# Optimization experiments

Hardware: AMD Instinct MI355X
Metric: run time of the kernel (lower is better)

Reference implementation:

```python
import jax, jax.numpy as jnp
import numpy as np

B, D = 65536, 1024
E, U, T = 10, 10, 2  # experts, expert units, tasks


def setup_inputs() -> dict:
    key = jax.random.key(0)
    ks = jax.random.split(key, 8)
    s = 0.02
    return {
        "x": jax.random.normal(ks[0], (B, D), dtype=jnp.float32),
        "show_index": jax.random.randint(ks[1], (B,), 0, 100),
        "st": jax.random.normal(ks[2], (B, 16), dtype=jnp.float32),
        "expert_w": jax.random.normal(ks[3], (E, D, U), dtype=jnp.float32) * s,
        "expert_b": jnp.zeros((E, U), dtype=jnp.float32),
        "gate_w": jax.random.normal(ks[4], (T, D, E), dtype=jnp.float32) * s,
        "gate_b": jnp.zeros((T, E), dtype=jnp.float32),
        "ctr_w": jax.random.normal(ks[5], (U, 1), dtype=jnp.float32) * s,
        "ctr_b": jnp.zeros((1,), dtype=jnp.float32),
        "cvr_w": jax.random.normal(ks[6], (U, 1), dtype=jnp.float32) * s,
        "cvr_b": jnp.zeros((1,), dtype=jnp.float32),
    }


def reference(x, show_index, st, expert_w, expert_b, gate_w, gate_b,
              ctr_w, ctr_b, cvr_w, cvr_b):
    # experts_output[b, u, e] = relu(x @ W_e + b_e)  (stacked on axis 2)
    experts_output = jax.nn.relu(
        jnp.einsum("bd,edu->bue", x, expert_w) + expert_b.T[None, :, :]
    )  # [B, U, E]
    # gates[b, t, e] = softmax over experts
    gates = jax.nn.softmax(
        jnp.einsum("bd,tde->bte", x, gate_w) + gate_b[None, :, :], axis=-1
    )  # [B, T, E]
    # weighted sum over experts for each task: [B, T, U]
    task_inputs = jnp.einsum("bue,bte->btu", experts_output, gates)
    ctr_logits = jax.nn.sigmoid(task_inputs[:, 0, :] @ ctr_w + ctr_b)  # [B, 1]
    cvr_logits = jax.nn.sigmoid(task_inputs[:, 1, :] @ cvr_w + cvr_b)  # [B, 1]
    return (ctr_logits, cvr_logits)
```

## Files before the change

### kernel.cpp

```cpp
#include <hip/hip_runtime.h>
#include <hip/hip_bf16.h>

#define B_ROWS 65536
#define D_DIM  1024
#define NC     120
#define NCP    128
#define MBLK   64
#define BK     64
#define ASTR   72
#define CSTR   121

typedef __attribute__((ext_vector_type(4))) float f32x4;
typedef __attribute__((ext_vector_type(8))) short bf16x8;

__device__ __forceinline__ unsigned short f2bf(float f) {
  union { float f; unsigned u; } v; v.f = f;
  unsigned r = v.u + 0x7FFFu + ((v.u >> 16) & 1u);
  return (unsigned short)(r >> 16);
}

__global__ __launch_bounds__(256) void pack_w(const float* __restrict__ ew,
                                              const float* __restrict__ gw,
                                              short* __restrict__ wt) {
  int idx = blockIdx.x * 256 + threadIdx.x;
  int c = idx >> 10, d = idx & 1023;
  float v = 0.f;
  if (c < 100) {
    int e = c / 10, u = c % 10;
    v = ew[(e * D_DIM + d) * 10 + u];
  } else if (c < NC) {
    int q = c - 100; int t = q / 10, e = q % 10;
    v = gw[(t * D_DIM + d) * 10 + e];
  }
  wt[c * D_DIM + d] = (short)f2bf(v);
}

union Smem {
  struct { short A[MBLK * ASTR]; short Bm[NCP * ASTR]; } s;
  float C[MBLK * CSTR];
};

__global__ __launch_bounds__(256) void mmoe_main(
    const float* __restrict__ x, const short* __restrict__ wt,
    const float* __restrict__ eb, const float* __restrict__ gb,
    const float* __restrict__ ctr_w, const float* __restrict__ ctr_b,
    const float* __restrict__ cvr_w, const float* __restrict__ cvr_b,
    float* __restrict__ out) {
  __shared__ Smem sm;
  const int tid  = threadIdx.x;
  const int wave = tid >> 6, lane = tid & 63;
  const int m0   = blockIdx.x * MBLK;

  const int arow = tid >> 4;
  const int akp  = (tid & 15) * 4;
  const int bc   = tid >> 3;
  const int bks  = (tid & 7) * 8;

  const int lhi = lane >> 4;
  const int llo = lane & 15;

  f32x4 acc[8];
  const f32x4 vzero = {0.f, 0.f, 0.f, 0.f};
  #pragma unroll
  for (int i = 0; i < 8; ++i) acc[i] = vzero;

  for (int k0 = 0; k0 < D_DIM; k0 += BK) {
    __syncthreads();
    #pragma unroll
    for (int j = 0; j < 4; ++j) {
      const int row = j * 16 + arow;
      const float4 v = *reinterpret_cast<const float4*>(
          x + (size_t)(m0 + row) * D_DIM + k0 + akp);
      ushort4 h;
      h.x = f2bf(v.x); h.y = f2bf(v.y); h.z = f2bf(v.z); h.w = f2bf(v.w);
      *reinterpret_cast<ushort4*>(&sm.s.A[row * ASTR + akp]) = h;
    }
    #pragma unroll
    for (int j = 0; j < 4; ++j) {
      const int c = j * 32 + bc;
      const uint4 v = *reinterpret_cast<const uint4*>(wt + c * D_DIM + k0 + bks);
      *reinterpret_cast<uint4*>(&sm.s.Bm[c * ASTR + bks]) = v;
    }
    __syncthreads();
    #pragma unroll
    for (int ks = 0; ks < BK; ks += 32) {
      const bf16x8 af = *reinterpret_cast<const bf16x8*>(
          &sm.s.A[(wave * 16 + llo) * ASTR + ks + lhi * 8]);
      #pragma unroll
      for (int ct = 0; ct < 8; ++ct) {
        const bf16x8 bf = *reinterpret_cast<const bf16x8*>(
            &sm.s.Bm[(ct * 16 + llo) * ASTR + ks + lhi * 8]);
        acc[ct] = __builtin_amdgcn_mfma_f32_16x16x32_bf16(af, bf, acc[ct], 0, 0, 0);
      }
    }
  }

  __syncthreads();
  #pragma unroll
  for (int ct = 0; ct < 8; ++ct) {
    const int col = ct * 16 + llo;
    if (col < NC) {
      #pragma unroll
      for (int r = 0; r < 4; ++r) {
        const int row = wave * 16 + lhi * 4 + r;
        sm.C[row * CSTR + col] = acc[ct][r];
      }
    }
  }
  __syncthreads();

  if (tid < MBLK) {
    const float* crow = &sm.C[tid * CSTR];
    float w0[10], w1[10];
    #pragma unroll
    for (int u = 0; u < 10; ++u) { w0[u] = ctr_w[u]; w1[u] = cvr_w[u]; }
    float s0[10], s1[10];
    #pragma unroll
    for (int e = 0; e < 10; ++e) {
      float a0 = 0.f, a1 = 0.f;
      #pragma unroll
      for (int u = 0; u < 10; ++u) {
        float v = crow[e * 10 + u] + eb[e * 10 + u];
        v = fmaxf(v, 0.f);
        a0 = fmaf(v, w0[u], a0);
        a1 = fmaf(v, w1[u], a1);
      }
      s0[e] = a0; s1[e] = a1;
    }
    {
      float gl[10], mx = -1e30f;
      #pragma unroll
      for (int e = 0; e < 10; ++e) { gl[e] = crow[100 + e] + gb[e]; mx = fmaxf(mx, gl[e]); }
      float den = 0.f, num = 0.f;
      #pragma unroll
      for (int e = 0; e < 10; ++e) {
        float p = __expf(gl[e] - mx); den += p; num = fmaf(p, s0[e], num);
      }
      float z = num / den + ctr_b[0];
      out[m0 + tid] = 1.f / (1.f + __expf(-z));
    }
    {
      float gl[10], mx = -1e30f;
      #pragma unroll
      for (int e = 0; e < 10; ++e) { gl[e] = crow[110 + e] + gb[10 + e]; mx = fmaxf(mx, gl[e]); }
      float den = 0.f, num = 0.f;
      #pragma unroll
      for (int e = 0; e < 10; ++e) {
        float p = __expf(gl[e] - mx); den += p; num = fmaf(p, s1[e], num);
      }
      float z = num / den + cvr_b[0];
      out[B_ROWS + m0 + tid] = 1.f / (1.f + __expf(-z));
    }
  }
}

extern "C" void kernel_launch(void* const* d_in, const int* in_sizes, int n_in,
                              void* d_out, int out_size, void* d_ws, size_t ws_size,
                              hipStream_t stream) {
  const float* x     = (const float*)d_in[0];
  const float* ew    = (const float*)d_in[3];
  const float* eb    = (const float*)d_in[4];
  const float* gw    = (const float*)d_in[5];
  const float* gb    = (const float*)d_in[6];
  const float* ctr_w = (const float*)d_in[7];
  const float* ctr_b = (const float*)d_in[8];
  const float* cvr_w = (const float*)d_in[9];
  const float* cvr_b = (const float*)d_in[10];
  float* out = (float*)d_out;
  short* wt  = (short*)d_ws;

  pack_w<<<512, 256, 0, stream>>>(ew, gw, wt);
  mmoe_main<<<B_ROWS / MBLK, 256, 0, stream>>>(x, wt, eb, gb, ctr_w, ctr_b,
                                               cvr_w, cvr_b, out);
}
```

Measured before the change: 399.1 us.

## Double-buffer weight tiles via direct global-to-LDS loads and register-prefetch x

Restructures the main GEMM loop so the A operand (x) is loaded straight into registers in MFMA fragment layout and converted to bf16 there, which removes the LDS staging for x. The packed weights are streamed with global_load_lds into a double-buffered, XOR-swizzled LDS tile, and the next chunk is prefetched while the current one is computed, with one barrier per chunk. The epilogue is split across 128 threads, one per task, and launch bounds request 4 blocks per CU. The intent is to hide global memory latency and cut LDS traffic on this memory-bound kernel, at the cost of more registers for the prefetch buffers.

```diff
diff --git a/kernel.cpp b/kernel.cpp
--- a/kernel.cpp
+++ b/kernel.cpp
@@ -4,10 +4,7 @@
 #define B_ROWS 65536
 #define D_DIM  1024
 #define NC     120
-#define NCP    128
 #define MBLK   64
-#define BK     64
-#define ASTR   72
 #define CSTR   121
 
 typedef __attribute__((ext_vector_type(4))) float f32x4;
@@ -17,6 +14,12 @@
   union { float f; unsigned u; } v; v.f = f;
   unsigned r = v.u + 0x7FFFu + ((v.u >> 16) & 1u);
   return (unsigned short)(r >> 16);
+}
+
+__device__ __forceinline__ void gload_lds16(const short* g, short* l) {
+  __builtin_amdgcn_global_load_lds(
+      (const __attribute__((address_space(1))) void*)g,
+      (__attribute__((address_space(3))) void*)l, 16, 0, 0);
 }
 
 __global__ __launch_bounds__(256) void pack_w(const float* __restrict__ ew,
@@ -36,11 +39,11 @@
 }
 
 union Smem {
-  struct { short A[MBLK * ASTR]; short Bm[NCP * ASTR]; } s;
+  short Bq[2][8192];
   float C[MBLK * CSTR];
 };
 
-__global__ __launch_bounds__(256) void mmoe_main(
+__global__ __launch_bounds__(256, 4) void mmoe_main(
     const float* __restrict__ x, const short* __restrict__ wt,
     const float* __restrict__ eb, const float* __restrict__ gb,
     const float* __restrict__ ctr_w, const float* __restrict__ ctr_b,
@@ -49,108 +52,117 @@
   __shared__ Smem sm;
   const int tid  = threadIdx.x;
   const int wave = tid >> 6, lane = tid & 63;
+  const int lhi  = lane >> 4, llo = lane & 15;
   const int m0   = blockIdx.x * MBLK;
 
-  const int arow = tid >> 4;
-  const int akp  = (tid & 15) * 4;
-  const int bc   = tid >> 3;
-  const int bks  = (tid & 7) * 8;
-
-  const int lhi = lane >> 4;
-  const int llo = lane & 15;
+  const float* xrow = x + (size_t)(m0 + wave * 16 + llo) * D_DIM + lhi * 8;
 
   f32x4 acc[8];
-  const f32x4 vzero = {0.f, 0.f, 0.f, 0.f};
   #pragma unroll
-  for (int i = 0; i < 8; ++i) acc[i] = vzero;
+  for (int i = 0; i < 8; ++i) acc[i] = (f32x4){0.f, 0.f, 0.f, 0.f};
 
-  for (int k0 = 0; k0 < D_DIM; k0 += BK) {
-    __syncthreads();
+  float4 pa[2][4];
+
+  #pragma unroll
+  for (int j = 0; j < 4; ++j) {
+    const int slot = j * 256 + wave * 64 + lane;
+    const int c = slot >> 3, p = slot & 7;
+    const int g = p ^ (c & 7);
+    gload_lds16(wt + c * D_DIM + g * 8,
+                &sm.Bq[0][(j * 256 + wave * 64) * 8]);
+  }
+  pa[0][0] = *(const float4*)(xrow + 0);
+  pa[0][1] = *(const float4*)(xrow + 4);
+  pa[0][2] = *(const float4*)(xrow + 32);
+  pa[0][3] = *(const float4*)(xrow + 36);
+  __syncthreads();
+
+  for (int ch = 0; ch < 16; ++ch) {
+    const int cur = ch & 1;
+    if (ch < 15) {
+      const int k1 = (ch + 1) * 64;
+      #pragma unroll
+      for (int j = 0; j < 4; ++j) {
+        const int slot = j * 256 + wave * 64 + lane;
+        const int c = slot >> 3, p = slot & 7;
+        const int g = p ^ (c & 7);
+        gload_lds16(wt + c * D_DIM + k1 + g * 8,
+                    &sm.Bq[cur ^ 1][(j * 256 + wave * 64) * 8]);
+      }
+      pa[cur ^ 1][0] = *(const float4*)(xrow + k1);
+      pa[cur ^ 1][1] = *(const float4*)(xrow + k1 + 4);
+      pa[cur ^ 1][2] = *(const float4*)(xrow + k1 + 32);
+      pa[cur ^ 1][3] = *(const float4*)(xrow + k1 + 36);
+    }
+    bf16x8 af0, af1;
+    {
+      const float4 a = pa[cur][0], b = pa[cur][1];
+      af0[0] = (short)f2bf(a.x); af0[1] = (short)f2bf(a.y);
+      af0[2] = (short)f2bf(a.z); af0[3] = (short)f2bf(a.w);
+      af0[4] = (short)f2bf(b.x); af0[5] = (short)f2bf(b.y);
+      af0[6] = (short)f2bf(b.z); af0[7] = (short)f2bf(b.w);
+      const float4 c2 = pa[cur][2], d2 = pa[cur][3];
+      af1[0] = (short)f2bf(c2.x); af1[1] = (short)f2bf(c2.y);
+      af1[2] = (short)f2bf(c2.z); af1[3] = (short)f2bf(c2.w);
+      af1[4] = (short)f2bf(d2.x); af1[5] = (short)f2bf(d2.y);
+      af1[6] = (short)f2bf(d2.z); af1[7] = (short)f2bf(d2.w);
+    }
+    const int swz = llo & 7;
     #pragma unroll
-    for (int j = 0; j < 4; ++j) {
-      const int row = j * 16 + arow;
-      const float4 v = *reinterpret_cast<const float4*>(
-          x + (size_t)(m0 + row) * D_DIM + k0 + akp);
-      ushort4 h;
-      h.x = f2bf(v.x); h.y = f2bf(v.y); h.z = f2bf(v.z); h.w = f2bf(v.w);
-      *reinterpret_cast<ushort4*>(&sm.s.A[row * ASTR + akp]) = h;
-    }
-    #pragma unroll
-    for (int j = 0; j < 4; ++j) {
-      const int c = j * 32 + bc;
-      const uint4 v = *reinterpret_cast<const uint4*>(wt + c * D_DIM + k0 + bks);
-      *reinterpret_cast<uint4*>(&sm.s.Bm[c * ASTR + bks]) = v;
+    for (int half = 0; half < 2; ++half) {
+      const bf16x8 a = half ? af1 : af0;
+      const int g0 = half * 4 + lhi;
+      const int p  = g0 ^ swz;
+      #pragma unroll
+      for (int ct = 0; ct < 8; ++ct) {
+        const bf16x8 bfr = *(const bf16x8*)&sm.Bq[cur][(ct * 16 + llo) * 64 + p * 8];
+        acc[ct] = __builtin_amdgcn_mfma_f32_16x16x32_bf16(a, bfr, acc[ct], 0, 0, 0);
+      }
     }
     __syncthreads();
-    #pragma unroll
-    for (int ks = 0; ks < BK; ks += 32) {
-      const bf16x8 af = *reinterpret_cast<const bf16x8*>(
-          &sm.s.A[(wave * 16 + llo) * ASTR + ks + lhi * 8]);
-      #pragma unroll
-      for (int ct = 0; ct < 8; ++ct) {
-        const bf16x8 bf = *reinterpret_cast<const bf16x8*>(
-            &sm.s.Bm[(ct * 16 + llo) * ASTR + ks + lhi * 8]);
-        acc[ct] = __builtin_amdgcn_mfma_f32_16x16x32_bf16(af, bf, acc[ct], 0, 0, 0);
-      }
-    }
   }
 
-  __syncthreads();
   #pragma unroll
   for (int ct = 0; ct < 8; ++ct) {
     const int col = ct * 16 + llo;
     if (col < NC) {
       #pragma unroll
-      for (int r = 0; r < 4; ++r) {
-        const int row = wave * 16 + lhi * 4 + r;
-        sm.C[row * CSTR + col] = acc[ct][r];
-      }
+      for (int r = 0; r < 4; ++r)
+        sm.C[(wave * 16 + lhi * 4 + r) * CSTR + col] = acc[ct][r];
     }
   }
   __syncthreads();
 
-  if (tid < MBLK) {
-    const float* crow = &sm.C[tid * CSTR];
-    float w0[10], w1[10];
-    #pragma unroll
-    for (int u = 0; u < 10; ++u) { w0[u] = ctr_w[u]; w1[u] = cvr_w[u]; }
-    float s0[10], s1[10];
+  if (tid < 128) {
+    const int task = tid >> 6, row = tid & 63;
+    const float* crow = &sm.C[row * CSTR];
+    const float* tw = task ? cvr_w : ctr_w;
+    const float tb = task ? cvr_b[0] : ctr_b[0];
+    float s[10];
     #pragma unroll
     for (int e = 0; e < 10; ++e) {
-      float a0 = 0.f, a1 = 0.f;
+      float a = 0.f;
       #pragma unroll
       for (int u = 0; u < 10; ++u) {
-        float v = crow[e * 10 + u] + eb[e * 10 + u];
-        v = fmaxf(v, 0.f);
-        a0 = fmaf(v, w0[u], a0);
-        a1 = fmaf(v, w1[u], a1);
+        float v = fmaxf(crow[e * 10 + u] + eb[e * 10 + u], 0.f);
+        a = fmaf(v, tw[u], a);
       }
-      s0[e] = a0; s1[e] = a1;
+      s[e] = a;
     }
-    {
-      float gl[10], mx = -1e30f;
-      #pragma unroll
-      for (int e = 0; e < 10; ++e) { gl[e] = crow[100 + e] + gb[e]; mx = fmaxf(mx, gl[e]); }
-      float den = 0.f, num = 0.f;
-      #pragma unroll
-      for (int e = 0; e < 10; ++e) {
-        float p = __expf(gl[e] - mx); den += p; num = fmaf(p, s0[e], num);
-      }
-      float z = num / den + ctr_b[0];
-      out[m0 + tid] = 1.f / (1.f + __expf(-z));
+    float gl[10], mx = -1e30f;
+    #pragma unroll
+    for (int e = 0; e < 10; ++e) {
+      gl[e] = crow[100 + task * 10 + e] + gb[task * 10 + e];
+      mx = fmaxf(mx, gl[e]);
     }
-    {
-      float gl[10], mx = -1e30f;
-      #pragma unroll
-      for (int e = 0; e < 10; ++e) { gl[e] = crow[110 + e] + gb[10 + e]; mx = fmaxf(mx, gl[e]); }
-      float den = 0.f, num = 0.f;
-      #pragma unroll
-      for (int e = 0; e < 10; ++e) {
-        float p = __expf(gl[e] - mx); den += p; num = fmaf(p, s1[e], num);
-      }
-      float z = num / den + cvr_b[0];
-      out[B_ROWS + m0 + tid] = 1.f / (1.f + __expf(-z));
+    float den = 0.f, num = 0.f;
+    #pragma unroll
+    for (int e = 0; e < 10; ++e) {
+      float pz = __expf(gl[e] - mx);
+      den += pz; num = fmaf(pz, s[e], num);
     }
+    const float z = num / den + tb;
+    out[task * B_ROWS + m0 + row] = 1.f / (1.f + __expf(-z));
   }
 }
 
```

After: 412.9 us. 3.4% more time.
